# Kernel optimization log

Measured on AMD Instinct MI355X. Metric: run time of the kernel, lower is better.

## Reference

```python
import jax, jax.numpy as jnp
import numpy as np

N_NODES = 100000
N_EDGES = 1600000
D_IN = 128
D_OUT = 128


def setup_inputs() -> dict:
    key = jax.random.key(0)
    k1, k2, k3, k4, k5, k6 = jax.random.split(key, 6)
    x = jax.random.normal(k1, (N_NODES, D_IN), dtype=jnp.float32)
    edge_row = jax.random.randint(k2, (N_EDGES,), 0, N_NODES, dtype=jnp.int64)
    edge_col = jax.random.randint(k3, (N_EDGES,), 0, N_NODES, dtype=jnp.int64)
    edge_val = jax.random.uniform(k4, (N_EDGES,), dtype=jnp.float32)
    # Xavier-uniform init for weight, zeros for bias (matches reset_parameters)
    limit = float(np.sqrt(6.0 / (D_IN + D_OUT)))
    weight = jax.random.uniform(k5, (D_IN, D_OUT), minval=-limit, maxval=limit, dtype=jnp.float32)
    bias = jax.random.normal(k6, (D_OUT,), dtype=jnp.float32) * 0.02
    return {"x": x, "edge_row": edge_row, "edge_col": edge_col,
            "edge_val": edge_val, "weight": weight, "bias": bias}


def reference(x, edge_row, edge_col, edge_val, weight, bias):
    # dropout(p=0.0) is identity in eval -> omitted
    support = x @ weight                       # [N, D_OUT] dense GEMM
    # SpMM: out[r] = sum_{e: row[e]==r} val[e] * support[col[e]]
    messages = edge_val[:, None] * support[edge_col]   # [E, D_OUT]
    out = jax.ops.segment_sum(messages, edge_row, num_segments=N_NODES)
    return out + bias
```

## Files before the change

kernel.cpp:

```cpp
#include <hip/hip_runtime.h>


#define DMODEL 128
#define CAP 56
#define BROWS 128
#define BSHIFT 7
#define BCAP 2560
#define NB_SC 256
#define SC_THREADS 1024
#define SC_EPT 8
#define MAXBUCK 800
#define CURPAD 16

typedef __attribute__((ext_vector_type(8))) short short8_t;
typedef __attribute__((ext_vector_type(4))) float float4_t;

__device__ inline short f2bf(float f) {
    unsigned u = __float_as_uint(f);
    return (short)((u + 0x7FFFu + ((u >> 16) & 1u)) >> 16);
}

__global__ __launch_bounds__(256) void prep_kernel(const float* __restrict__ w,
                                                   unsigned short* __restrict__ wsw,
                                                   int* __restrict__ cursor, int n_cursor) {
    if (blockIdx.x < 8) {
        int c = blockIdx.x * 256 + threadIdx.x;
        int lane = c & 63;
        int kcnt = c >> 6;
        int kc = kcnt & 3, nt = kcnt >> 2;
        int n  = nt * 16 + (lane & 15);
        int k0 = kc * 32 + (lane >> 4) * 8;
        short8_t v;
        #pragma unroll
        for (int j = 0; j < 8; ++j)
            v[j] = f2bf(w[(size_t)(k0 + j) * DMODEL + n]);
        *(short8_t*)&wsw[(size_t)c * 8] = v;
    } else {
        for (int j = threadIdx.x; j < n_cursor; j += 256) cursor[j] = 0;
    }
}

__global__ __launch_bounds__(SC_THREADS) void scatter_kernel(
    const int* __restrict__ erow, const int* __restrict__ ecol,
    const float* __restrict__ eval,
    int* __restrict__ cursor, uint2* __restrict__ rec, int n_edges, int nbuck)
{
    __shared__ int cnt[MAXBUCK];
    __shared__ int gb[MAXBUCK];
    for (int j = threadIdx.x; j < nbuck; j += SC_THREADS) cnt[j] = 0;
    __syncthreads();

    int chunk = (n_edges + (int)gridDim.x - 1) / (int)gridDim.x;
    int base  = blockIdx.x * chunk;
    int lim   = n_edges - base; if (lim > chunk) lim = chunk;

    int lr[SC_EPT];
    #pragma unroll
    for (int i = 0; i < SC_EPT; ++i) {
        int idx = (int)threadIdx.x + i * SC_THREADS;
        lr[i] = -1;
        if (idx < lim) {
            int b = erow[base + idx] >> BSHIFT;
            lr[i] = atomicAdd(&cnt[b], 1);
        }
    }
    __syncthreads();
    for (int j = threadIdx.x; j < nbuck; j += SC_THREADS) {
        int c = cnt[j];
        gb[j] = c ? atomicAdd(&cursor[j * CURPAD], c) : 0;
    }
    __syncthreads();
    #pragma unroll
    for (int i = 0; i < SC_EPT; ++i) {
        if (lr[i] >= 0) {
            int e = base + (int)threadIdx.x + i * SC_THREADS;
            int r = erow[e];
            int b = r >> BSHIFT;
            int pos = gb[b] + lr[i];
            if (pos < BCAP) {
                unsigned q = (unsigned)(eval[e] * 32767.0f + 0.5f);
                uint2 v;
                v.x = (q << 17) | (unsigned)ecol[e];
                v.y = (unsigned)(r & (BROWS - 1));
                rec[(size_t)b * BCAP + pos] = v;
            }
        }
    }
}

__global__ __launch_bounds__(256) void gemm_kernel(
    const float* __restrict__ x, const unsigned short* __restrict__ wsw,
    unsigned short* __restrict__ support, int n_nodes)
{
    int wv   = threadIdx.x >> 6;
    int lane = threadIdx.x & 63;
    int m    = lane & 15;
    int g    = lane >> 4;

    int rowA  = blockIdx.x * 64 + wv * 16 + m;
    int rowAc = rowA < n_nodes ? rowA : n_nodes - 1;
    const float* xr = x + (size_t)rowAc * DMODEL + g * 8;

    short8_t af[4];
    #pragma unroll
    for (int kc = 0; kc < 4; ++kc) {
        float4 u0 = *(const float4*)(xr + kc * 32);
        float4 u1 = *(const float4*)(xr + kc * 32 + 4);
        short8_t a;
        a[0] = f2bf(u0.x); a[1] = f2bf(u0.y); a[2] = f2bf(u0.z); a[3] = f2bf(u0.w);
        a[4] = f2bf(u1.x); a[5] = f2bf(u1.y); a[6] = f2bf(u1.z); a[7] = f2bf(u1.w);
        af[kc] = a;
    }

    const short8_t* wf = (const short8_t*)wsw;

    float4_t acc[8];
    #pragma unroll
    for (int nt = 0; nt < 8; ++nt) {
        float4_t z = {0.f, 0.f, 0.f, 0.f};
        acc[nt] = z;
        #pragma unroll
        for (int kc = 0; kc < 4; ++kc) {
            short8_t bf = wf[(nt * 4 + kc) * 64 + lane];
            acc[nt] = __builtin_amdgcn_mfma_f32_16x16x32_bf16(af[kc], bf, acc[nt], 0, 0, 0);
        }
    }

    int orow = blockIdx.x * 64 + wv * 16 + g * 4;
    #pragma unroll
    for (int r = 0; r < 4; ++r) {
        int row = orow + r;
        if (row < n_nodes) {
            #pragma unroll
            for (int nt = 0; nt < 8; ++nt)
                support[(size_t)row * DMODEL + nt * 16 + m] = (unsigned short)f2bf(acc[nt][r]);
        }
    }
}

__global__ __launch_bounds__(256) void bucket_aggregate_kernel(
    const int* __restrict__ cursor, const uint2* __restrict__ rec,
    const uint4* __restrict__ sup, const float* __restrict__ bias,
    float* __restrict__ out, int n_nodes)
{
    int b = blockIdx.x;
    __shared__ unsigned grouped[BROWS * CAP];
    __shared__ int cnt[BROWS];
    for (int j = threadIdx.x; j < BROWS; j += 256) cnt[j] = 0;
    __syncthreads();

    int cb = cursor[b * CURPAD]; if (cb > BCAP) cb = BCAP;
    const uint2* rb = rec + (size_t)b * BCAP;
    for (int j = threadIdx.x; j < cb; j += 256) {
        uint2 v = rb[j];
        int rl = (int)v.y;
        int rk = atomicAdd(&cnt[rl], 1);
        if (rk < CAP) grouped[rl * CAP + rk] = v.x;
    }
    __syncthreads();

    int wv   = threadIdx.x >> 6;
    int lane = threadIdx.x & 63;
    int sub  = lane >> 4;
    int q    = lane & 15;

    const float SCL = 1.0f / 32767.0f;

    for (int nl = wv * 32; nl < wv * 32 + 32; ++nl) {
        int node = (b << BSHIFT) + nl;
        if (node >= n_nodes) break;
        int len = cnt[nl];
        if (len > CAP) len = CAP;
        const unsigned* ed = &grouped[nl * CAP];

        float acc[8];
        #pragma unroll
        for (int k = 0; k < 8; ++k) acc[k] = 0.f;

        #define EDGE_FMA(rec_, p)                                                \
            {                                                                    \
                float v = (float)((rec_) >> 17) * SCL;                           \
                acc[0] = fmaf(v, __uint_as_float((p).x << 16), acc[0]);          \
                acc[1] = fmaf(v, __uint_as_float((p).x & 0xFFFF0000u), acc[1]);  \
                acc[2] = fmaf(v, __uint_as_float((p).y << 16), acc[2]);          \
                acc[3] = fmaf(v, __uint_as_float((p).y & 0xFFFF0000u), acc[3]);  \
                acc[4] = fmaf(v, __uint_as_float((p).z << 16), acc[4]);          \
                acc[5] = fmaf(v, __uint_as_float((p).z & 0xFFFF0000u), acc[5]);  \
                acc[6] = fmaf(v, __uint_as_float((p).w << 16), acc[6]);          \
                acc[7] = fmaf(v, __uint_as_float((p).w & 0xFFFF0000u), acc[7]);  \
            }

        int i = sub;
        for (; i + 12 < len; i += 16) {
            unsigned r0 = ed[i];
            unsigned r1 = ed[i + 4];
            unsigned r2 = ed[i + 8];
            unsigned r3 = ed[i + 12];
            uint4 p0 = sup[(size_t)(r0 & 0x1FFFFu) * 16 + q];
            uint4 p1 = sup[(size_t)(r1 & 0x1FFFFu) * 16 + q];
            uint4 p2 = sup[(size_t)(r2 & 0x1FFFFu) * 16 + q];
            uint4 p3 = sup[(size_t)(r3 & 0x1FFFFu) * 16 + q];
            EDGE_FMA(r0, p0);
            EDGE_FMA(r1, p1);
            EDGE_FMA(r2, p2);
            EDGE_FMA(r3, p3);
        }
        for (; i < len; i += 4) {
            unsigned r0 = ed[i];
            uint4 p0 = sup[(size_t)(r0 & 0x1FFFFu) * 16 + q];
            EDGE_FMA(r0, p0);
        }
        #undef EDGE_FMA

        #pragma unroll
        for (int k = 0; k < 8; ++k) {
            acc[k] += __shfl_xor(acc[k], 16);
            acc[k] += __shfl_xor(acc[k], 32);
        }

        if (sub == 0) {
            float4 b0 = ((const float4*)bias)[q * 2];
            float4 b1 = ((const float4*)bias)[q * 2 + 1];
            float4_t o0 = {acc[0] + b0.x, acc[1] + b0.y, acc[2] + b0.z, acc[3] + b0.w};
            float4_t o1 = {acc[4] + b1.x, acc[5] + b1.y, acc[6] + b1.z, acc[7] + b1.w};
            __builtin_nontemporal_store(o0, (float4_t*)out + (size_t)node * 32 + q * 2);
            __builtin_nontemporal_store(o1, (float4_t*)out + (size_t)node * 32 + q * 2 + 1);
        }
    }
}

extern "C" void kernel_launch(void* const* d_in, const int* in_sizes, int n_in,
                              void* d_out, int out_size, void* d_ws, size_t ws_size,
                              hipStream_t stream) {
    const float* x      = (const float*)d_in[0];
    const int*   erow   = (const int*)d_in[1];
    const int*   ecol   = (const int*)d_in[2];
    const float* eval   = (const float*)d_in[3];
    const float* weight = (const float*)d_in[4];
    const float* bias   = (const float*)d_in[5];
    float* out = (float*)d_out;

    const int n_nodes = in_sizes[0] / DMODEL;
    const int n_edges = in_sizes[3];
    const int nbuck   = (n_nodes + BROWS - 1) / BROWS;

    char* ws = (char*)d_ws;
    unsigned short* support = (unsigned short*)ws;  ws += (size_t)n_nodes * DMODEL * 2;
    unsigned short* wsw     = (unsigned short*)ws;  ws += (size_t)DMODEL * DMODEL * 2;
    int*      cursor = (int*)ws;                    ws += ((size_t)nbuck * CURPAD * 4 + 63) & ~63ull;
    uint2*    rec    = (uint2*)ws;                  ws += (size_t)nbuck * BCAP * 8;

    const int nb_g = (n_nodes + 63) / 64;
    const int n_cursor = nbuck * CURPAD;

    prep_kernel<<<9, 256, 0, stream>>>(weight, wsw, cursor, n_cursor);
    scatter_kernel<<<NB_SC, SC_THREADS, 0, stream>>>(erow, ecol, eval, cursor, rec, n_edges, nbuck);
    gemm_kernel<<<nb_g, 256, 0, stream>>>(x, wsw, support, n_nodes);
    bucket_aggregate_kernel<<<nbuck, 256, 0, stream>>>(
        cursor, rec, (const uint4*)support, bias, out, n_nodes);
}
```

Baseline: 233.0 us.

## Fuse GEMM and edge scatter into one launch, widen aggregate blocks

Merges the bucket-scatter kernel and the bf16 MFMA GEMM into one grid. The first nb_g blocks compute support and the trailing 256 blocks scatter edges, so the two independent phases can overlap and one launch is dropped. The scatter blocks shrink from 1024 to 256 threads and replace per-thread register ranks with a second shared-memory atomic counter, which adds atomics and a second read of erow. The aggregate kernel moves to 512 threads, so each wave handles 16 nodes instead of 32, raising parallelism per bucket.

```diff
diff --git a/kernel.cpp b/kernel.cpp
--- a/kernel.cpp
+++ b/kernel.cpp
@@ -7,8 +7,6 @@
 #define BSHIFT 7
 #define BCAP 2560
 #define NB_SC 256
-#define SC_THREADS 1024
-#define SC_EPT 8
 #define MAXBUCK 800
 #define CURPAD 16
 
@@ -40,43 +38,41 @@
     }
 }
 
-__global__ __launch_bounds__(SC_THREADS) void scatter_kernel(
+__global__ __launch_bounds__(256) void fused_gemm_scatter(
+    const float* __restrict__ x, const unsigned short* __restrict__ wsw,
+    unsigned short* __restrict__ support,
     const int* __restrict__ erow, const int* __restrict__ ecol,
     const float* __restrict__ eval,
-    int* __restrict__ cursor, uint2* __restrict__ rec, int n_edges, int nbuck)
+    int* __restrict__ cursor, uint2* __restrict__ rec,
+    int n_nodes, int n_edges, int nb_g, int nbuck)
 {
     __shared__ int cnt[MAXBUCK];
     __shared__ int gb[MAXBUCK];
-    for (int j = threadIdx.x; j < nbuck; j += SC_THREADS) cnt[j] = 0;
-    __syncthreads();
-
-    int chunk = (n_edges + (int)gridDim.x - 1) / (int)gridDim.x;
-    int base  = blockIdx.x * chunk;
-    int lim   = n_edges - base; if (lim > chunk) lim = chunk;
-
-    int lr[SC_EPT];
-    #pragma unroll
-    for (int i = 0; i < SC_EPT; ++i) {
-        int idx = (int)threadIdx.x + i * SC_THREADS;
-        lr[i] = -1;
-        if (idx < lim) {
-            int b = erow[base + idx] >> BSHIFT;
-            lr[i] = atomicAdd(&cnt[b], 1);
-        }
-    }
-    __syncthreads();
-    for (int j = threadIdx.x; j < nbuck; j += SC_THREADS) {
-        int c = cnt[j];
-        gb[j] = c ? atomicAdd(&cursor[j * CURPAD], c) : 0;
-    }
-    __syncthreads();
-    #pragma unroll
-    for (int i = 0; i < SC_EPT; ++i) {
-        if (lr[i] >= 0) {
-            int e = base + (int)threadIdx.x + i * SC_THREADS;
+    __shared__ int cnt2[MAXBUCK];
+
+    if ((int)blockIdx.x >= nb_g) {
+        int sb = blockIdx.x - nb_g;
+        for (int j = threadIdx.x; j < nbuck; j += 256) { cnt[j] = 0; cnt2[j] = 0; }
+        __syncthreads();
+
+        int chunk = (n_edges + NB_SC - 1) / NB_SC;
+        int base  = sb * chunk;
+        int lim   = n_edges - base; if (lim > chunk) lim = chunk;
+
+        for (int idx = threadIdx.x; idx < lim; idx += 256)
+            atomicAdd(&cnt[erow[base + idx] >> BSHIFT], 1);
+        __syncthreads();
+        for (int j = threadIdx.x; j < nbuck; j += 256) {
+            int c = cnt[j];
+            gb[j] = c ? atomicAdd(&cursor[j * CURPAD], c) : 0;
+        }
+        __syncthreads();
+        for (int idx = threadIdx.x; idx < lim; idx += 256) {
+            int e = base + idx;
             int r = erow[e];
             int b = r >> BSHIFT;
-            int pos = gb[b] + lr[i];
+            int rk = atomicAdd(&cnt2[b], 1);
+            int pos = gb[b] + rk;
             if (pos < BCAP) {
                 unsigned q = (unsigned)(eval[e] * 32767.0f + 0.5f);
                 uint2 v;
@@ -85,13 +81,9 @@
                 rec[(size_t)b * BCAP + pos] = v;
             }
         }
-    }
-}
-
-__global__ __launch_bounds__(256) void gemm_kernel(
-    const float* __restrict__ x, const unsigned short* __restrict__ wsw,
-    unsigned short* __restrict__ support, int n_nodes)
-{
+        return;
+    }
+
     int wv   = threadIdx.x >> 6;
     int lane = threadIdx.x & 63;
     int m    = lane & 15;
@@ -138,7 +130,7 @@
     }
 }
 
-__global__ __launch_bounds__(256) void bucket_aggregate_kernel(
+__global__ __launch_bounds__(512) void bucket_aggregate_kernel(
     const int* __restrict__ cursor, const uint2* __restrict__ rec,
     const uint4* __restrict__ sup, const float* __restrict__ bias,
     float* __restrict__ out, int n_nodes)
@@ -146,12 +138,12 @@
     int b = blockIdx.x;
     __shared__ unsigned grouped[BROWS * CAP];
     __shared__ int cnt[BROWS];
-    for (int j = threadIdx.x; j < BROWS; j += 256) cnt[j] = 0;
+    for (int j = threadIdx.x; j < BROWS; j += 512) cnt[j] = 0;
     __syncthreads();
 
     int cb = cursor[b * CURPAD]; if (cb > BCAP) cb = BCAP;
     const uint2* rb = rec + (size_t)b * BCAP;
-    for (int j = threadIdx.x; j < cb; j += 256) {
+    for (int j = threadIdx.x; j < cb; j += 512) {
         uint2 v = rb[j];
         int rl = (int)v.y;
         int rk = atomicAdd(&cnt[rl], 1);
@@ -166,7 +158,7 @@
 
     const float SCL = 1.0f / 32767.0f;
 
-    for (int nl = wv * 32; nl < wv * 32 + 32; ++nl) {
+    for (int nl = wv * 16; nl < wv * 16 + 16; ++nl) {
         int node = (b << BSHIFT) + nl;
         if (node >= n_nodes) break;
         int len = cnt[nl];
@@ -254,8 +246,8 @@
     const int n_cursor = nbuck * CURPAD;
 
     prep_kernel<<<9, 256, 0, stream>>>(weight, wsw, cursor, n_cursor);
-    scatter_kernel<<<NB_SC, SC_THREADS, 0, stream>>>(erow, ecol, eval, cursor, rec, n_edges, nbuck);
-    gemm_kernel<<<nb_g, 256, 0, stream>>>(x, wsw, support, n_nodes);
-    bucket_aggregate_kernel<<<nbuck, 256, 0, stream>>>(
+    fused_gemm_scatter<<<nb_g + NB_SC, 256, 0, stream>>>(
+        x, wsw, support, erow, ecol, eval, cursor, rec, n_nodes, n_edges, nb_g, nbuck);
+    bucket_aggregate_kernel<<<nbuck, 512, 0, stream>>>(
         cursor, rec, (const uint4*)support, bias, out, n_nodes);
 }
```

Measured after the change: 264.5 us. 13.5% more time.

## Fuse edge scatter and dense GEMM into one launch, widen aggregate blocks

Applied to the files above, without the earlier changes.

Scatter and GEMM now run as one 1024-thread kernel: the first 256 blocks bucket the edges and the remaining blocks each compute 256 rows of the bf16 support matrix. This lets the two independent stages overlap on the GPU and removes one launch. Cursor zeroing moves from the prep kernel to a hipMemsetAsync. The aggregate kernel now uses 512 threads, so each wave handles 16 nodes instead of 32. The 1024-thread launch bound may limit registers for the GEMM path, and the larger aggregate blocks change occupancy.

```diff
diff --git a/kernel.cpp b/kernel.cpp
--- a/kernel.cpp
+++ b/kernel.cpp
@@ -7,10 +7,10 @@
 #define BSHIFT 7
 #define BCAP 2560
 #define NB_SC 256
-#define SC_THREADS 1024
 #define SC_EPT 8
 #define MAXBUCK 800
 #define CURPAD 16
+#define GROWS 256
 
 typedef __attribute__((ext_vector_type(8))) short short8_t;
 typedef __attribute__((ext_vector_type(4))) float float4_t;
@@ -21,83 +21,81 @@
 }
 
 __global__ __launch_bounds__(256) void prep_kernel(const float* __restrict__ w,
-                                                   unsigned short* __restrict__ wsw,
-                                                   int* __restrict__ cursor, int n_cursor) {
-    if (blockIdx.x < 8) {
-        int c = blockIdx.x * 256 + threadIdx.x;
-        int lane = c & 63;
-        int kcnt = c >> 6;
-        int kc = kcnt & 3, nt = kcnt >> 2;
-        int n  = nt * 16 + (lane & 15);
-        int k0 = kc * 32 + (lane >> 4) * 8;
-        short8_t v;
-        #pragma unroll
-        for (int j = 0; j < 8; ++j)
-            v[j] = f2bf(w[(size_t)(k0 + j) * DMODEL + n]);
-        *(short8_t*)&wsw[(size_t)c * 8] = v;
-    } else {
-        for (int j = threadIdx.x; j < n_cursor; j += 256) cursor[j] = 0;
-    }
-}
-
-__global__ __launch_bounds__(SC_THREADS) void scatter_kernel(
+                                                   unsigned short* __restrict__ wsw) {
+    int c = blockIdx.x * 256 + threadIdx.x;
+    int lane = c & 63;
+    int kcnt = c >> 6;
+    int kc = kcnt & 3, nt = kcnt >> 2;
+    int n  = nt * 16 + (lane & 15);
+    int k0 = kc * 32 + (lane >> 4) * 8;
+    short8_t v;
+    #pragma unroll
+    for (int j = 0; j < 8; ++j)
+        v[j] = f2bf(w[(size_t)(k0 + j) * DMODEL + n]);
+    *(short8_t*)&wsw[(size_t)c * 8] = v;
+}
+
+__global__ __launch_bounds__(1024) void fused_scatter_gemm(
+    const float* __restrict__ x, const unsigned short* __restrict__ wsw,
+    unsigned short* __restrict__ support,
     const int* __restrict__ erow, const int* __restrict__ ecol,
     const float* __restrict__ eval,
-    int* __restrict__ cursor, uint2* __restrict__ rec, int n_edges, int nbuck)
+    int* __restrict__ cursor, uint2* __restrict__ rec,
+    int n_nodes, int n_edges, int nbuck)
 {
     __shared__ int cnt[MAXBUCK];
-    __shared__ int gb[MAXBUCK];
-    for (int j = threadIdx.x; j < nbuck; j += SC_THREADS) cnt[j] = 0;
-    __syncthreads();
-
-    int chunk = (n_edges + (int)gridDim.x - 1) / (int)gridDim.x;
-    int base  = blockIdx.x * chunk;
-    int lim   = n_edges - base; if (lim > chunk) lim = chunk;
-
-    int lr[SC_EPT];
-    #pragma unroll
-    for (int i = 0; i < SC_EPT; ++i) {
-        int idx = (int)threadIdx.x + i * SC_THREADS;
-        lr[i] = -1;
-        if (idx < lim) {
-            int b = erow[base + idx] >> BSHIFT;
-            lr[i] = atomicAdd(&cnt[b], 1);
-        }
-    }
-    __syncthreads();
-    for (int j = threadIdx.x; j < nbuck; j += SC_THREADS) {
-        int c = cnt[j];
-        gb[j] = c ? atomicAdd(&cursor[j * CURPAD], c) : 0;
-    }
-    __syncthreads();
-    #pragma unroll
-    for (int i = 0; i < SC_EPT; ++i) {
-        if (lr[i] >= 0) {
-            int e = base + (int)threadIdx.x + i * SC_THREADS;
-            int r = erow[e];
-            int b = r >> BSHIFT;
-            int pos = gb[b] + lr[i];
-            if (pos < BCAP) {
-                unsigned q = (unsigned)(eval[e] * 32767.0f + 0.5f);
-                uint2 v;
-                v.x = (q << 17) | (unsigned)ecol[e];
-                v.y = (unsigned)(r & (BROWS - 1));
-                rec[(size_t)b * BCAP + pos] = v;
+    __shared__ int gbase[MAXBUCK];
+
+    if ((int)blockIdx.x < NB_SC) {
+        for (int j = threadIdx.x; j < nbuck; j += 1024) cnt[j] = 0;
+        __syncthreads();
+
+        int chunk = (n_edges + NB_SC - 1) / NB_SC;
+        int base  = blockIdx.x * chunk;
+        int lim   = n_edges - base; if (lim > chunk) lim = chunk;
+
+        int lr[SC_EPT];
+        #pragma unroll
+        for (int i = 0; i < SC_EPT; ++i) {
+            int idx = (int)threadIdx.x + i * 1024;
+            lr[i] = -1;
+            if (idx < lim) {
+                int b = erow[base + idx] >> BSHIFT;
+                lr[i] = atomicAdd(&cnt[b], 1);
             }
         }
-    }
-}
-
-__global__ __launch_bounds__(256) void gemm_kernel(
-    const float* __restrict__ x, const unsigned short* __restrict__ wsw,
-    unsigned short* __restrict__ support, int n_nodes)
-{
+        __syncthreads();
+        for (int j = threadIdx.x; j < nbuck; j += 1024) {
+            int c = cnt[j];
+            gbase[j] = c ? atomicAdd(&cursor[j * CURPAD], c) : 0;
+        }
+        __syncthreads();
+        #pragma unroll
+        for (int i = 0; i < SC_EPT; ++i) {
+            if (lr[i] >= 0) {
+                int e = base + (int)threadIdx.x + i * 1024;
+                int r = erow[e];
+                int b = r >> BSHIFT;
+                int pos = gbase[b] + lr[i];
+                if (pos < BCAP) {
+                    unsigned q = (unsigned)(eval[e] * 32767.0f + 0.5f);
+                    uint2 v;
+                    v.x = (q << 17) | (unsigned)ecol[e];
+                    v.y = (unsigned)(r & (BROWS - 1));
+                    rec[(size_t)b * BCAP + pos] = v;
+                }
+            }
+        }
+        return;
+    }
+
+    int tb   = blockIdx.x - NB_SC;
     int wv   = threadIdx.x >> 6;
     int lane = threadIdx.x & 63;
     int m    = lane & 15;
     int g    = lane >> 4;
 
-    int rowA  = blockIdx.x * 64 + wv * 16 + m;
+    int rowA  = tb * GROWS + wv * 16 + m;
     int rowAc = rowA < n_nodes ? rowA : n_nodes - 1;
     const float* xr = x + (size_t)rowAc * DMODEL + g * 8;
 
@@ -126,7 +124,7 @@
         }
     }
 
-    int orow = blockIdx.x * 64 + wv * 16 + g * 4;
+    int orow = tb * GROWS + wv * 16 + g * 4;
     #pragma unroll
     for (int r = 0; r < 4; ++r) {
         int row = orow + r;
@@ -138,7 +136,7 @@
     }
 }
 
-__global__ __launch_bounds__(256) void bucket_aggregate_kernel(
+__global__ __launch_bounds__(512) void bucket_aggregate_kernel(
     const int* __restrict__ cursor, const uint2* __restrict__ rec,
     const uint4* __restrict__ sup, const float* __restrict__ bias,
     float* __restrict__ out, int n_nodes)
@@ -146,12 +144,12 @@
     int b = blockIdx.x;
     __shared__ unsigned grouped[BROWS * CAP];
     __shared__ int cnt[BROWS];
-    for (int j = threadIdx.x; j < BROWS; j += 256) cnt[j] = 0;
+    for (int j = threadIdx.x; j < BROWS; j += 512) cnt[j] = 0;
     __syncthreads();
 
     int cb = cursor[b * CURPAD]; if (cb > BCAP) cb = BCAP;
     const uint2* rb = rec + (size_t)b * BCAP;
-    for (int j = threadIdx.x; j < cb; j += 256) {
+    for (int j = threadIdx.x; j < cb; j += 512) {
         uint2 v = rb[j];
         int rl = (int)v.y;
         int rk = atomicAdd(&cnt[rl], 1);
@@ -166,7 +164,7 @@
 
     const float SCL = 1.0f / 32767.0f;
 
-    for (int nl = wv * 32; nl < wv * 32 + 32; ++nl) {
+    for (int nl = wv * 16; nl < wv * 16 + 16; ++nl) {
         int node = (b << BSHIFT) + nl;
         if (node >= n_nodes) break;
         int len = cnt[nl];
@@ -250,12 +248,13 @@
     int*      cursor = (int*)ws;                    ws += ((size_t)nbuck * CURPAD * 4 + 63) & ~63ull;
     uint2*    rec    = (uint2*)ws;                  ws += (size_t)nbuck * BCAP * 8;
 
-    const int nb_g = (n_nodes + 63) / 64;
+    const int nb_g = (n_nodes + GROWS - 1) / GROWS;
     const int n_cursor = nbuck * CURPAD;
 
-    prep_kernel<<<9, 256, 0, stream>>>(weight, wsw, cursor, n_cursor);
-    scatter_kernel<<<NB_SC, SC_THREADS, 0, stream>>>(erow, ecol, eval, cursor, rec, n_edges, nbuck);
-    gemm_kernel<<<nb_g, 256, 0, stream>>>(x, wsw, support, n_nodes);
-    bucket_aggregate_kernel<<<nbuck, 256, 0, stream>>>(
+    hipMemsetAsync(cursor, 0, (size_t)n_cursor * sizeof(int), stream);
+    prep_kernel<<<8, 256, 0, stream>>>(weight, wsw);
+    fused_scatter_gemm<<<NB_SC + nb_g, 1024, 0, stream>>>(
+        x, wsw, support, erow, ecol, eval, cursor, rec, n_nodes, n_edges, nbuck);
+    bucket_aggregate_kernel<<<nbuck, 512, 0, stream>>>(
         cursor, rec, (const uint4*)support, bias, out, n_nodes);
 }
```

Result: slower. 240.9 us (+3.4%).
